# Kernel optimization log

Hardware: AMD Instinct MI355X
Metric: run time of the kernel (lower is better)

## Reference

```python
import jax, jax.numpy as jnp
import numpy as np

N_EXPERT = 8
TOP_K = 2
NEG_INF = -1e9  # finite sentinel so softmax grads stay well-defined


def setup_inputs() -> dict:
    key = jax.random.key(0)
    ks = jax.random.split(key, 8)
    B, S, D, F, E = 2, 2048, 1024, 4096, N_EXPERT
    sd = 1.0 / np.sqrt(D)
    sf = 1.0 / np.sqrt(F)
    return {
        "x": jax.random.normal(ks[0], (B, S, D), jnp.float32),
        "noise": jax.random.normal(ks[1], (B, S, E), jnp.float32),
        "Wr": jax.random.normal(ks[2], (D, E), jnp.float32) * sd,
        "br": jnp.zeros((E,), jnp.float32),
        "Wn": jax.random.normal(ks[3], (D, E), jnp.float32) * sd,
        "bn": jnp.zeros((E,), jnp.float32),
        "W1": jax.random.normal(ks[4], (E, D, F), jnp.float32) * sd,
        "b1": jnp.zeros((E, F), jnp.float32),
        "W2": jax.random.normal(ks[5], (E, F, D), jnp.float32) * sf,
        "b2": jnp.zeros((E, D), jnp.float32),
    }


def reference(x, noise, Wr, br, Wn, bn, W1, b1, W2, b2):
    # NoisyTopkRouter: logits + noise * softplus(noise_logits)
    logits = jnp.einsum("bsd,de->bse", x, Wr) + br
    noise_logits = jnp.einsum("bsd,de->bse", x, Wn) + bn
    noisy = logits + noise * jax.nn.softplus(noise_logits)

    # keep only top-k logits, -inf elsewhere, softmax over experts
    _, top_ids = jax.lax.top_k(noisy, TOP_K)                  # [B,S,K]
    sel = jnp.sum(jax.nn.one_hot(top_ids, N_EXPERT, dtype=noisy.dtype), axis=-2) > 0  # [B,S,E]
    gates = jax.nn.softmax(jnp.where(sel, noisy, NEG_INF), axis=-1)  # zeros off top-k

    # Expert MLP: Linear -> ReLU -> Linear (dropout = 0 at inference).
    # Gates are exactly zero for non-selected experts, so the dense einsum
    # combine equals the original masked gather/scatter-add.
    h = jax.nn.relu(jnp.einsum("bsd,edf->ebsf", x, W1) + b1[:, None, None, :])
    eo = jnp.einsum("ebsf,efd->ebsd", h, W2) + b2[:, None, None, :]
    return jnp.einsum("bse,ebsd->bsd", gates, eo)
```

## Files before the change

kernel.cpp:

```cpp
#include <hip/hip_runtime.h>

#define T_TOK 4096
#define DDIM 1024
#define FDIM 4096
#define NE 8
#define NPAIR 8192
#define MAXT128 72

typedef short bf16x8 __attribute__((ext_vector_type(8)));
typedef float f32x4 __attribute__((ext_vector_type(4)));

__device__ inline unsigned short f2bf(float f) {
  union { float f; unsigned u; } a; a.f = f;
  unsigned r = a.u + 0x7fffu + ((a.u >> 16) & 1u);
  return (unsigned short)(r >> 16);
}

__device__ __forceinline__ void gload16(const void* g, void* l) {
  __builtin_amdgcn_global_load_lds(
      (const __attribute__((address_space(1))) unsigned int*)g,
      (__attribute__((address_space(3))) unsigned int*)l, 16, 0, 0);
}

__global__ __launch_bounds__(256) void router_kernel(
    const float* __restrict__ x, const float* __restrict__ noise,
    const float* __restrict__ Wr, const float* __restrict__ br,
    const float* __restrict__ Wn, const float* __restrict__ bn,
    int* __restrict__ tok_top, float* __restrict__ tok_gate,
    ushort* __restrict__ xb)
{
  int t = blockIdx.x * 4 + (threadIdx.x >> 6);
  int lane = threadIdx.x & 63;
  const float* xr = x + (size_t)t * DDIM;
  ushort* xo = xb + (size_t)t * DDIM;
  float accR[NE] = {}, accN[NE] = {};
  for (int d = lane; d < DDIM; d += 64) {
    float xv = xr[d];
    xo[d] = f2bf(xv);
    const float* wr = Wr + (size_t)d * NE;
    const float* wn = Wn + (size_t)d * NE;
#pragma unroll
    for (int e = 0; e < NE; ++e) {
      accR[e] = fmaf(xv, wr[e], accR[e]);
      accN[e] = fmaf(xv, wn[e], accN[e]);
    }
  }
#pragma unroll
  for (int off = 32; off > 0; off >>= 1) {
#pragma unroll
    for (int e = 0; e < NE; ++e) {
      accR[e] += __shfl_xor(accR[e], off);
      accN[e] += __shfl_xor(accN[e], off);
    }
  }
  if (lane == 0) {
    float noisy[NE];
#pragma unroll
    for (int e = 0; e < NE; ++e) {
      float lg = accR[e] + br[e];
      float nl = accN[e] + bn[e];
      float sp = fmaxf(nl, 0.f) + log1pf(expf(-fabsf(nl)));
      noisy[e] = lg + noise[(size_t)t * NE + e] * sp;
    }
    int e0 = 0;
#pragma unroll
    for (int e = 1; e < NE; ++e) if (noisy[e] > noisy[e0]) e0 = e;
    int e1 = (e0 == 0) ? 1 : 0;
#pragma unroll
    for (int e = 0; e < NE; ++e)
      if (e != e0 && e != e1 && noisy[e] > noisy[e1]) e1 = e;
    float v0 = noisy[e0], v1 = noisy[e1];
    float ex = __expf(v1 - v0);
    float inv = 1.f / (1.f + ex);
    tok_top[t * 2] = e0; tok_top[t * 2 + 1] = e1;
    tok_gate[t * 2] = inv; tok_gate[t * 2 + 1] = ex * inv;
  }
}

__global__ __launch_bounds__(256) void scan_scatter_kernel(
    const int* __restrict__ tok_top, int* __restrict__ off, int* __restrict__ tiles,
    int* __restrict__ pair_tok, int* __restrict__ tok_ppos)
{
  __shared__ int smat[NE][256];
  __shared__ int tot[NE];
  __shared__ int loff[NE];
  int tid = threadIdx.x;
  int c[NE] = {};
  for (int i = 0; i < 16; ++i) {
    int t = tid * 16 + i;
    int e0 = tok_top[2 * t], e1 = tok_top[2 * t + 1];
#pragma unroll
    for (int e = 0; e < NE; ++e) c[e] += (e0 == e) + (e1 == e);
  }
#pragma unroll
  for (int e = 0; e < NE; ++e) smat[e][tid] = c[e];
  __syncthreads();
  if (tid < NE) {
    int s = 0;
    for (int j = 0; j < 256; ++j) { int v = smat[tid][j]; smat[tid][j] = s; s += v; }
    tot[tid] = s;
  }
  __syncthreads();
  if (tid == 0) {
    int s = 0, nt = 0;
    for (int e = 0; e < NE; ++e) {
      loff[e] = s; off[e] = s;
      int tt = (tot[e] + 127) >> 7;
      for (int m = 0; m < tt; ++m) tiles[1 + nt++] = (e << 8) | m;
      s += tot[e];
    }
    off[NE] = s;
    tiles[0] = nt;
  }
  __syncthreads();
  for (int i = 0; i < 16; ++i) {
    int t = tid * 16 + i;
#pragma unroll
    for (int k = 0; k < 2; ++k) {
      int e = tok_top[2 * t + k];
      int pos = loff[e] + smat[e][tid];
      smat[e][tid] = smat[e][tid] + 1;
      pair_tok[pos] = t;
      tok_ppos[2 * t + k] = pos;
    }
  }
}

__global__ __launch_bounds__(256) void transpose_bf_kernel(
    const float* __restrict__ W1, const float* __restrict__ W2,
    ushort* __restrict__ WT1, ushort* __restrict__ WT2)
{
  __shared__ float tile[64][65];
  int z = blockIdx.z;
  const float* src; ushort* dst; int R, C, bx, by;
  if (z < NE) {
    src = W1 + (size_t)z * DDIM * FDIM; dst = WT1 + (size_t)z * FDIM * DDIM;
    R = DDIM; C = FDIM; bx = blockIdx.x; by = blockIdx.y;
  } else {
    src = W2 + (size_t)(z - NE) * FDIM * DDIM; dst = WT2 + (size_t)(z - NE) * DDIM * FDIM;
    R = FDIM; C = DDIM; bx = blockIdx.y; by = blockIdx.x;
  }
  int c0 = bx * 64, r0 = by * 64;
  int tid = threadIdx.x;
  int tr = tid >> 4;
  int tc4 = (tid & 15) * 4;
#pragma unroll
  for (int i = 0; i < 64; i += 16) {
    float4 v = *(const float4*)(src + (size_t)(r0 + tr + i) * C + c0 + tc4);
    tile[tr + i][tc4] = v.x; tile[tr + i][tc4 + 1] = v.y;
    tile[tr + i][tc4 + 2] = v.z; tile[tr + i][tc4 + 3] = v.w;
  }
  __syncthreads();
  int cc = tid >> 4;
  int rr4 = (tid & 15) * 4;
#pragma unroll
  for (int i = 0; i < 64; i += 16) {
    int c = cc + i;
    ushort4 o;
    o.x = f2bf(tile[rr4][c]); o.y = f2bf(tile[rr4 + 1][c]);
    o.z = f2bf(tile[rr4 + 2][c]); o.w = f2bf(tile[rr4 + 3][c]);
    *(ushort4*)(dst + (size_t)(c0 + c) * R + r0 + rr4) = o;
  }
}

template<int KD, int ND, int EPI, int INDIR>
__global__ __launch_bounds__(256) void gemm4_kernel(
    const ushort* __restrict__ A, const ushort* __restrict__ BT,
    const int* __restrict__ off, const int* __restrict__ tiles,
    const int* __restrict__ pair_tok, const float* __restrict__ bias,
    ushort* __restrict__ Hout, float* __restrict__ EOout)
{
  constexpr int GX = ND / 128;
  constexpr int NKT = KD / 64;
  __shared__ __align__(16) ushort As[128 * 64];
  __shared__ __align__(16) ushort Bs[128 * 64];

  int total = tiles[0] * GX;
  int orig = blockIdx.x + GX * (int)blockIdx.y;
  if (orig >= total) return;
  int q = total >> 3, r = total & 7, xcd = orig & 7, idx = orig >> 3;
  int wg = (xcd < r ? xcd * (q + 1) : r * (q + 1) + (xcd - r) * q) + idx;
  int ti = wg / GX, bx = wg - ti * GX;

  int te = tiles[1 + ti];
  int e = te >> 8, mt = te & 255;
  int base = off[e];
  int cnt = off[e + 1] - base;
  int m0 = mt << 7, n0 = bx << 7;

  int tid = threadIdx.x, lane = tid & 63, wid = tid >> 6;
  int wr = wid >> 1, wc = wid & 1;

  int arow[4];
#pragma unroll
  for (int c = 0; c < 4; ++c) {
    int rl = (c * 256 + tid) >> 3;
    int mr = m0 + rl; if (mr >= cnt) mr = cnt - 1;
    arow[c] = INDIR ? pair_tok[base + mr] : base + mr;
  }
  const char* Ab = (const char*)A;
  const char* Bgb = (const char*)(BT + ((size_t)e * ND + n0) * KD);

  f32x4 acc[4][4] = {};

  for (int t = 0; t < NKT; ++t) {
    __syncthreads();
    int kb = t * 128;
#pragma unroll
    for (int c = 0; c < 4; ++c) {
      int ch = c * 256 + tid;
      int row = ch >> 3, b = (ch & 7) * 16;
      gload16(Ab + (size_t)arow[c] * (KD * 2) + kb + (b ^ ((row & 7) << 4)),
              (char*)As + ch * 16);
    }
#pragma unroll
    for (int c = 0; c < 4; ++c) {
      int ch = c * 256 + tid;
      int row = ch >> 3, b = (ch & 7) * 16;
      gload16(Bgb + (size_t)row * (KD * 2) + kb + (b ^ ((row & 7) << 4)),
              (char*)Bs + ch * 16);
    }
    __syncthreads();

    bf16x8 af[4][2], bv[4][2];
#pragma unroll
    for (int m = 0; m < 4; ++m) {
      int row = wr * 64 + m * 16 + (lane & 15);
      int sw = (row & 7) << 4;
#pragma unroll
      for (int ks = 0; ks < 2; ++ks)
        af[m][ks] = *(const bf16x8*)((const char*)As + row * 128 +
                                     ((ks * 64 + (lane >> 4) * 16) ^ sw));
    }
#pragma unroll
    for (int n = 0; n < 4; ++n) {
      int row = wc * 64 + n * 16 + (lane & 15);
      int sw = (row & 7) << 4;
#pragma unroll
      for (int ks = 0; ks < 2; ++ks)
        bv[n][ks] = *(const bf16x8*)((const char*)Bs + row * 128 +
                                     ((ks * 64 + (lane >> 4) * 16) ^ sw));
    }
#pragma unroll
    for (int ks = 0; ks < 2; ++ks)
#pragma unroll
      for (int m = 0; m < 4; ++m)
#pragma unroll
        for (int n = 0; n < 4; ++n)
          acc[m][n] = __builtin_amdgcn_mfma_f32_16x16x32_bf16(
              af[m][ks], bv[n][ks], acc[m][n], 0, 0, 0);
  }

  float bvv[4];
#pragma unroll
  for (int n = 0; n < 4; ++n)
    bvv[n] = bias[(size_t)e * ND + n0 + wc * 64 + n * 16 + (lane & 15)];
  int rq = (lane >> 4) << 2;
#pragma unroll
  for (int m = 0; m < 4; ++m) {
#pragma unroll
    for (int qq = 0; qq < 4; ++qq) {
      int rr = m0 + wr * 64 + m * 16 + rq + qq;
      if (rr < cnt) {
#pragma unroll
        for (int n = 0; n < 4; ++n) {
          int col = n0 + wc * 64 + n * 16 + (lane & 15);
          float v = acc[m][n][qq] + bvv[n];
          if (EPI == 0) {
            v = fmaxf(v, 0.f);
            Hout[(size_t)(base + rr) * ND + col] = f2bf(v);
          } else {
            EOout[(size_t)(base + rr) * ND + col] = v;
          }
        }
      }
    }
  }
}

__global__ __launch_bounds__(256) void combine_kernel(
    const float* __restrict__ eo, const int* __restrict__ tok_ppos,
    const float* __restrict__ tok_gate, float* __restrict__ out)
{
  int t = blockIdx.x;
  int tid = threadIdx.x;
  int p0 = tok_ppos[t * 2], p1 = tok_ppos[t * 2 + 1];
  float g0 = tok_gate[t * 2], g1 = tok_gate[t * 2 + 1];
  float4 a = ((const float4*)(eo + (size_t)p0 * DDIM))[tid];
  float4 b = ((const float4*)(eo + (size_t)p1 * DDIM))[tid];
  float4 o;
  o.x = g0 * a.x + g1 * b.x;
  o.y = g0 * a.y + g1 * b.y;
  o.z = g0 * a.z + g1 * b.z;
  o.w = g0 * a.w + g1 * b.w;
  ((float4*)(out + (size_t)t * DDIM))[tid] = o;
}

extern "C" void kernel_launch(void* const* d_in, const int* in_sizes, int n_in,
                              void* d_out, int out_size, void* d_ws, size_t ws_size,
                              hipStream_t stream)
{
  const float* x     = (const float*)d_in[0];
  const float* noise = (const float*)d_in[1];
  const float* Wr    = (const float*)d_in[2];
  const float* br    = (const float*)d_in[3];
  const float* Wn    = (const float*)d_in[4];
  const float* bn    = (const float*)d_in[5];
  const float* W1    = (const float*)d_in[6];
  const float* b1    = (const float*)d_in[7];
  const float* W2    = (const float*)d_in[8];
  const float* b2    = (const float*)d_in[9];
  float* out = (float*)d_out;

  char* ws = (char*)d_ws;
  size_t o = 0;
  auto alloc = [&](size_t sz) {
    void* p = ws + o;
    o = (o + sz + 255) & ~(size_t)255;
    return p;
  };
  ushort* WT1 = (ushort*)alloc((size_t)NE * FDIM * DDIM * 2);
  ushort* WT2 = (ushort*)alloc((size_t)NE * DDIM * FDIM * 2);
  ushort* XB  = (ushort*)alloc((size_t)T_TOK * DDIM * 2);
  ushort* H   = (ushort*)alloc((size_t)(NPAIR + 256) * FDIM * 2);
  float*  EO  = (float*)alloc((size_t)(NPAIR + 256) * DDIM * 4);
  int*    TOK_TOP  = (int*)alloc(T_TOK * 2 * 4);
  float*  TOK_GATE = (float*)alloc(T_TOK * 2 * 4);
  int*    TOK_PPOS = (int*)alloc(T_TOK * 2 * 4);
  int*    PAIR_TOK = (int*)alloc((NPAIR + 256) * 4);
  int*    OFF = (int*)alloc(64);
  int*    TILES = (int*)alloc((1 + MAXT128) * 4);

  router_kernel<<<T_TOK / 4, 256, 0, stream>>>(x, noise, Wr, br, Wn, bn,
                                               TOK_TOP, TOK_GATE, XB);
  scan_scatter_kernel<<<1, 256, 0, stream>>>(TOK_TOP, OFF, TILES, PAIR_TOK, TOK_PPOS);
  transpose_bf_kernel<<<dim3(64, 16, 16), 256, 0, stream>>>(W1, W2, WT1, WT2);
  gemm4_kernel<DDIM, FDIM, 0, 1>
      <<<dim3(FDIM / 128, MAXT128), 256, 0, stream>>>(XB, WT1, OFF, TILES, PAIR_TOK, b1, H, nullptr);
  gemm4_kernel<FDIM, DDIM, 1, 0>
      <<<dim3(DDIM / 128, MAXT128), 256, 0, stream>>>(H, WT2, OFF, TILES, PAIR_TOK, b2, nullptr, EO);
  combine_kernel<<<T_TOK, 256, 0, stream>>>(EO, TOK_PPOS, TOK_GATE, out);
}
```

Before: 324.4 us.

## Double-buffer LDS tiles in grouped expert GEMM to overlap loads with MFMA

Replaces the single-buffered A/B shared tiles with two 32KB stages, so the next K-slice is loaded with global_load_lds while MFMAs run on the current one. One barrier per iteration now uses explicit vmcnt/lgkmcnt waits instead of two __syncthreads. It also precomputes per-thread global pointers and LDS read offsets to cut address arithmetic. LDS use doubles to 64KB per block, which may lower occupancy.

```diff
diff --git a/kernel.cpp b/kernel.cpp
--- a/kernel.cpp
+++ b/kernel.cpp
@@ -172,8 +172,7 @@
 {
   constexpr int GX = ND / 128;
   constexpr int NKT = KD / 64;
-  __shared__ __align__(16) ushort As[128 * 64];
-  __shared__ __align__(16) ushort Bs[128 * 64];
+  __shared__ __align__(16) char lds[2 * 32768];
 
   int total = tiles[0] * GX;
   int orig = blockIdx.x + GX * (int)blockIdx.y;
@@ -191,56 +190,68 @@
   int tid = threadIdx.x, lane = tid & 63, wid = tid >> 6;
   int wr = wid >> 1, wc = wid & 1;
 
-  int arow[4];
-#pragma unroll
-  for (int c = 0; c < 4; ++c) {
-    int rl = (c * 256 + tid) >> 3;
-    int mr = m0 + rl; if (mr >= cnt) mr = cnt - 1;
-    arow[c] = INDIR ? pair_tok[base + mr] : base + mr;
-  }
-  const char* Ab = (const char*)A;
-  const char* Bgb = (const char*)(BT + ((size_t)e * ND + n0) * KD);
-
-  f32x4 acc[4][4] = {};
-
-  for (int t = 0; t < NKT; ++t) {
-    __syncthreads();
-    int kb = t * 128;
+  const char* aptr[4];
+  const char* bptr[4];
+  {
+    const char* Ab = (const char*)A;
+    const char* Bgb = (const char*)(BT + ((size_t)e * ND + n0) * KD);
 #pragma unroll
     for (int c = 0; c < 4; ++c) {
       int ch = c * 256 + tid;
       int row = ch >> 3, b = (ch & 7) * 16;
-      gload16(Ab + (size_t)arow[c] * (KD * 2) + kb + (b ^ ((row & 7) << 4)),
-              (char*)As + ch * 16);
-    }
+      int bsw = b ^ ((row & 7) << 4);
+      int mr = m0 + row; if (mr >= cnt) mr = cnt - 1;
+      int ar = INDIR ? pair_tok[base + mr] : base + mr;
+      aptr[c] = Ab + (size_t)ar * (KD * 2) + bsw;
+      bptr[c] = Bgb + (size_t)row * (KD * 2) + bsw;
+    }
+  }
+
+  auto STAGE = [&](int bufi) {
+    char* d = lds + bufi * 32768;
 #pragma unroll
     for (int c = 0; c < 4; ++c) {
       int ch = c * 256 + tid;
-      int row = ch >> 3, b = (ch & 7) * 16;
-      gload16(Bgb + (size_t)row * (KD * 2) + kb + (b ^ ((row & 7) << 4)),
-              (char*)Bs + ch * 16);
-    }
-    __syncthreads();
-
+      gload16(aptr[c], d + ch * 16);
+      gload16(bptr[c], d + 16384 + ch * 16);
+      aptr[c] += 128;
+      bptr[c] += 128;
+    }
+  };
+
+  int lr = lane & 15, hi = lane >> 4;
+  int swl = (lane & 7) << 4;
+  int offA[2], offB[2];
+#pragma unroll
+  for (int ks = 0; ks < 2; ++ks) {
+    int kk = (ks * 64 + hi * 16) ^ swl;
+    offA[ks] = (wr * 64 + lr) * 128 + kk;
+    offB[ks] = (wc * 64 + lr) * 128 + kk;
+  }
+
+  f32x4 acc[4][4] = {};
+
+  STAGE(0);
+  asm volatile("s_waitcnt vmcnt(0)" ::: "memory");
+  __builtin_amdgcn_sched_barrier(0);
+  __builtin_amdgcn_s_barrier();
+
+  for (int t = 0; t < NKT; ++t) {
+    if (t + 1 < NKT) STAGE((t + 1) & 1);
+
+    const char* pa = lds + (t & 1) * 32768;
+    const char* pb = pa + 16384;
     bf16x8 af[4][2], bv[4][2];
 #pragma unroll
-    for (int m = 0; m < 4; ++m) {
-      int row = wr * 64 + m * 16 + (lane & 15);
-      int sw = (row & 7) << 4;
+    for (int m = 0; m < 4; ++m)
 #pragma unroll
       for (int ks = 0; ks < 2; ++ks)
-        af[m][ks] = *(const bf16x8*)((const char*)As + row * 128 +
-                                     ((ks * 64 + (lane >> 4) * 16) ^ sw));
-    }
-#pragma unroll
-    for (int n = 0; n < 4; ++n) {
-      int row = wc * 64 + n * 16 + (lane & 15);
-      int sw = (row & 7) << 4;
+        af[m][ks] = *(const bf16x8*)(pa + offA[ks] + m * 2048);
+#pragma unroll
+    for (int n = 0; n < 4; ++n)
 #pragma unroll
       for (int ks = 0; ks < 2; ++ks)
-        bv[n][ks] = *(const bf16x8*)((const char*)Bs + row * 128 +
-                                     ((ks * 64 + (lane >> 4) * 16) ^ sw));
-    }
+        bv[n][ks] = *(const bf16x8*)(pb + offB[ks] + n * 2048);
 #pragma unroll
     for (int ks = 0; ks < 2; ++ks)
 #pragma unroll
@@ -249,13 +260,18 @@
         for (int n = 0; n < 4; ++n)
           acc[m][n] = __builtin_amdgcn_mfma_f32_16x16x32_bf16(
               af[m][ks], bv[n][ks], acc[m][n], 0, 0, 0);
+
+    asm volatile("s_waitcnt lgkmcnt(0)" ::: "memory");
+    if (t + 1 < NKT) asm volatile("s_waitcnt vmcnt(0)" ::: "memory");
+    __builtin_amdgcn_sched_barrier(0);
+    __builtin_amdgcn_s_barrier();
   }
 
   float bvv[4];
 #pragma unroll
   for (int n = 0; n < 4; ++n)
-    bvv[n] = bias[(size_t)e * ND + n0 + wc * 64 + n * 16 + (lane & 15)];
-  int rq = (lane >> 4) << 2;
+    bvv[n] = bias[(size_t)e * ND + n0 + wc * 64 + n * 16 + lr];
+  int rq = hi << 2;
 #pragma unroll
   for (int m = 0; m < 4; ++m) {
 #pragma unroll
@@ -264,7 +280,7 @@
       if (rr < cnt) {
 #pragma unroll
         for (int n = 0; n < 4; ++n) {
-          int col = n0 + wc * 64 + n * 16 + (lane & 15);
+          int col = n0 + wc * 64 + n * 16 + lr;
           float v = acc[m][n][qq] + bvv[n];
           if (EPI == 0) {
             v = fmaxf(v, 0.f);
```

New measurement: 359.6 us. 10.9% more time.
